# Optimization experiments

Hardware: AMD Instinct MI355X
Metric: run time of the kernel (lower is better)

Reference implementation:

```python
import jax, jax.numpy as jnp
import numpy as np

N_NODES = 100000


def setup_inputs() -> dict:
    key = jax.random.key(0)
    ks = jax.random.split(key, 4)
    x = jax.random.normal(ks[0], (N_NODES, 64), dtype=jnp.float32)
    edge_index = jax.random.randint(ks[1], (2, 1600000), 0, N_NODES, dtype=jnp.int64)
    # Glorot-ish scaled weights
    W1 = jax.random.normal(ks[2], (64, 64), dtype=jnp.float32) * (1.0 / np.sqrt(64))
    b1 = jnp.zeros((64,), dtype=jnp.float32)
    W2 = jax.random.normal(ks[3], (64, 19), dtype=jnp.float32) * (1.0 / np.sqrt(64))
    b2 = jnp.zeros((19,), dtype=jnp.float32)
    return {"x": x, "edge_index": edge_index, "W1": W1, "b1": b1, "W2": W2, "b2": b2}


def _gcn_norm(edge_index, num_nodes, dtype):
    # PyG gcn_norm: add self-loops (fill_value=1, improved=False), then
    # norm = deg^-1/2[src] * deg^-1/2[dst] with deg computed over destination.
    loops = jnp.arange(num_nodes, dtype=edge_index.dtype)
    src = jnp.concatenate([edge_index[0], loops])
    dst = jnp.concatenate([edge_index[1], loops])
    deg = jax.ops.segment_sum(jnp.ones_like(dst, dtype=dtype), dst, num_segments=num_nodes)
    dinv = jax.lax.rsqrt(deg)  # deg >= 1 thanks to self-loops
    norm = dinv[src] * dinv[dst]  # [E + N]
    return src, dst, norm


def _gcn_conv(h, src, dst, norm, W, b, num_nodes):
    hw = h @ W                                  # dense transform [N, d_out]
    msg = norm[:, None] * hw[src]               # gather + edge scaling [E+N, d_out]
    out = jax.ops.segment_sum(msg, dst, num_segments=num_nodes)  # scatter-add
    return out + b


def reference(x, edge_index, W1, b1, W2, b2):
    n = x.shape[0]
    src, dst, norm = _gcn_norm(edge_index, n, x.dtype)
    h = jax.nn.relu(_gcn_conv(x, src, dst, norm, W1, b1, n))
    # dropout is identity in eval mode (training=False)
    return _gcn_conv(h, src, dst, norm, W2, b2, n)
```

## Files before the change

### kernel.cpp

```cpp
#include <hip/hip_runtime.h>

#define TPB 256
#define BSH 5
#define BNODES 32
#define CAP 1024
#define EPB 8192
#define NBMAX 3200


__global__ void k_hist1(const int* __restrict__ dst, int* __restrict__ hist,
                        int nb, int E) {
    __shared__ int sh[NBMAX];
    int tid = threadIdx.x, blk = blockIdx.x;
    for (int i = tid; i < nb; i += TPB) sh[i] = 0;
    __syncthreads();
    int e0 = blk * EPB;
    for (int i = tid; i < EPB; i += TPB) {
        int e = e0 + i;
        if (e < E) atomicAdd(&sh[dst[e] >> BSH], 1);
    }
    __syncthreads();
    int* hrow = hist + (size_t)blk * nb;
    for (int i = tid; i < nb; i += TPB) hrow[i] = sh[i];
}

__global__ void k_scanoff(const int* __restrict__ hist, int* __restrict__ offs,
                          int* __restrict__ bcnt, int nblk, int nb) {
    int t = blockIdx.x * TPB + threadIdx.x;
    int b = t >> 3, s = t & 7;
    if (b >= nb) return;
    int nps = (nblk + 7) >> 3;
    int sum = 0;
    for (int q = 0; q < nps; ++q) {
        int blk = q * 8 + s;
        if (blk < nblk) sum += hist[(size_t)blk * nb + b];
    }
    int v = sum;
#pragma unroll
    for (int o = 1; o < 8; o <<= 1) {
        int u = __shfl_up(v, o, 8);
        if (s >= o) v += u;
    }
    int total = __shfl(v, 7, 8);
    if (s == 0) bcnt[b] = total;
    int off = b * CAP + (v - sum);
    for (int q = 0; q < nps; ++q) {
        int blk = q * 8 + s;
        if (blk < nblk) {
            offs[(size_t)blk * nb + b] = off;
            off += hist[(size_t)blk * nb + b];
        }
    }
}

__global__ void k_scatter(const int* __restrict__ src, const int* __restrict__ dst,
                          const int* __restrict__ offs, unsigned* __restrict__ ebuf,
                          int nb, int E) {
    __shared__ int cur[NBMAX];
    int tid = threadIdx.x, blk = blockIdx.x;
    const int* orow = offs + (size_t)blk * nb;
    for (int i = tid; i < nb; i += TPB) cur[i] = orow[i];
    __syncthreads();
    int e0 = blk * EPB;
    for (int i = tid; i < EPB; i += TPB) {
        int e = e0 + i;
        if (e < E) {
            int d = dst[e];
            int pos = atomicAdd(&cur[d >> BSH], 1);
            ebuf[pos] = ((unsigned)src[e] << BSH) | (unsigned)(d & (BNODES - 1));
        }
    }
}

__global__ void k_bcsr(const int* __restrict__ bcnt, const unsigned* __restrict__ ebuf,
                       int* __restrict__ csr, int* __restrict__ node_beg,
                       int* __restrict__ degi, float* __restrict__ dinv, int nb, int n) {
    __shared__ unsigned se[4][CAP];
    __shared__ int scnt[4][BNODES];
    __shared__ int sexc[4][BNODES];
    __shared__ int srnk[4][BNODES];
    int wv = threadIdx.x >> 6, lane = threadIdx.x & 63;
    int b = blockIdx.x * 4 + wv;
    bool act = (b < nb);
    if (lane < BNODES) { scnt[wv][lane] = 0; srnk[wv][lane] = 0; }
    __syncthreads();
    int cnt = 0;
    if (act) {
        cnt = bcnt[b];
        if (cnt > CAP) cnt = CAP;
        const unsigned* p = &ebuf[(size_t)b * CAP];
        for (int k = lane; k < cnt; k += 64) {
            unsigned pk = p[k];
            se[wv][k] = pk;
            atomicAdd(&scnt[wv][pk & (BNODES - 1)], 1);
        }
    }
    __syncthreads();
    if (act && lane < BNODES) {
        int dg = scnt[wv][lane];
        int v = dg;
#pragma unroll
        for (int off = 1; off < BNODES; off <<= 1) {
            int t = __shfl_up(v, off, BNODES);
            if (lane >= off) v += t;
        }
        int excl = v - dg;
        sexc[wv][lane] = excl;
        int node = b * BNODES + lane;
        if (node < n) {
            degi[node] = dg;
            node_beg[node] = b * CAP + excl;
            dinv[node] = rsqrtf((float)dg + 1.0f);
        }
    }
    __syncthreads();
    if (act) {
        int* csrb = csr + (size_t)b * CAP;
        for (int k = lane; k < cnt; k += 64) {
            unsigned pk = se[wv][k];
            int dl = pk & (BNODES - 1);
            int r = atomicAdd(&srnk[wv][dl], 1);
            csrb[sexc[wv][dl] + r] = (int)(pk >> BSH);
        }
    }
}


__global__ void k_xw64v(const float* __restrict__ x, const float* __restrict__ W,
                        const float* __restrict__ dinv, _Float16* __restrict__ g, int n) {
    __shared__ float Ws[64 * 64];
    __shared__ float xsT[64 * 64];
    int tid = threadIdx.x;
    int row0 = blockIdx.x * 64;
    for (int i = tid; i < 1024; i += TPB)
        reinterpret_cast<float4*>(Ws)[i] = reinterpret_cast<const float4*>(W)[i];
    {
        int rl = tid >> 2, cq = (tid & 3) * 16;
        int row = row0 + rl;
#pragma unroll
        for (int j4 = 0; j4 < 4; ++j4) {
            float4 v = make_float4(0.f, 0.f, 0.f, 0.f);
            if (row < n) v = *reinterpret_cast<const float4*>(x + (size_t)row * 64 + cq + j4 * 4);
            xsT[(cq + j4 * 4 + 0) * 64 + rl] = v.x;
            xsT[(cq + j4 * 4 + 1) * 64 + rl] = v.y;
            xsT[(cq + j4 * 4 + 2) * 64 + rl] = v.z;
            xsT[(cq + j4 * 4 + 3) * 64 + rl] = v.w;
        }
    }
    __syncthreads();
    int c4 = (tid & 15) * 4, rq = (tid >> 4) * 4;
    float acc[4][4] = {};
#pragma unroll 4
    for (int k = 0; k < 64; ++k) {
        float4 wv = *reinterpret_cast<const float4*>(Ws + k * 64 + c4);
        float4 xv = *reinterpret_cast<const float4*>(xsT + k * 64 + rq);
        const float* wp = (const float*)&wv;
        const float* xp = (const float*)&xv;
#pragma unroll
        for (int i = 0; i < 4; ++i)
#pragma unroll
            for (int j = 0; j < 4; ++j) acc[i][j] += xp[i] * wp[j];
    }
#pragma unroll
    for (int i = 0; i < 4; ++i) {
        int row = row0 + rq + i;
        if (row < n) {
            float dv = dinv[row];
            _Float16 o[4];
#pragma unroll
            for (int j = 0; j < 4; ++j) o[j] = (_Float16)(dv * acc[i][j]);
            *reinterpret_cast<ushort4*>(g + (size_t)row * 64 + c4) =
                *reinterpret_cast<const ushort4*>(o);
        }
    }
}

__global__ void k_xw19v(const _Float16* __restrict__ h, const float* __restrict__ W,
                        const float* __restrict__ dinv, _Float16* __restrict__ g2, int n) {
    __shared__ float Ws[64 * 32];
    __shared__ float xsT[64 * 32];
    int tid = threadIdx.x;
    int row0 = blockIdx.x * 32;
    for (int i = tid; i < 64 * 32; i += TPB) {
        int k = i >> 5, c = i & 31;
        Ws[i] = (c < 19) ? W[k * 19 + c] : 0.f;
    }
    {
        int rl = tid >> 3, sq = tid & 7;
        int row = row0 + rl;
        if (row < n) {
            uint4 v = *(reinterpret_cast<const uint4*>(h + (size_t)row * 64) + sq);
            const _Float16* f = (const _Float16*)&v;
#pragma unroll
            for (int j = 0; j < 8; ++j) xsT[(sq * 8 + j) * 32 + rl] = (float)f[j];
        } else {
#pragma unroll
            for (int j = 0; j < 8; ++j) xsT[(sq * 8 + j) * 32 + rl] = 0.f;
        }
    }
    __syncthreads();
    int c = tid & 31, rg = (tid >> 5) * 4;
    float acc[4] = {};
#pragma unroll 4
    for (int k = 0; k < 64; ++k) {
        float wv = Ws[k * 32 + c];
        float4 xv = *reinterpret_cast<const float4*>(xsT + k * 32 + rg);
        const float* xp = (const float*)&xv;
#pragma unroll
        for (int i = 0; i < 4; ++i) acc[i] += xp[i] * wv;
    }
    if (c < 19) {
#pragma unroll
        for (int i = 0; i < 4; ++i) {
            int row = row0 + rg + i;
            if (row < n) g2[(size_t)row * 19 + c] = (_Float16)(dinv[row] * acc[i]);
        }
    }
}


__global__ void k_gath64d(const int* __restrict__ node_beg, const int* __restrict__ degi,
                          const int* __restrict__ csr, const float* __restrict__ dinv,
                          const _Float16* __restrict__ g, const float* __restrict__ b1,
                          _Float16* __restrict__ h, int n) {
    int node = blockIdx.x * 4 + (threadIdx.x >> 6);
    if (node >= n) return;
    int lane = threadIdx.x & 63;
    int eidx = lane >> 3, fch = lane & 7;
    int beg = node_beg[node], cnt = degi[node];
    const uint4* gb = (const uint4*)g;
    float acc[8];
#pragma unroll
    for (int j = 0; j < 8; ++j) acc[j] = 0.f;
    for (int base = 0; base < cnt; base += 32) {
        int k0 = base + eidx, k1 = base + 8 + eidx;
        int k2 = base + 16 + eidx, k3 = base + 24 + eidx;
        bool v0 = (k0 < cnt), v1 = (k1 < cnt), v2 = (k2 < cnt), v3 = (k3 < cnt);
        int r0 = v0 ? csr[beg + k0] : 0;
        int r1 = v1 ? csr[beg + k1] : 0;
        int r2 = v2 ? csr[beg + k2] : 0;
        int r3 = v3 ? csr[beg + k3] : 0;
        uint4 A = v0 ? gb[(size_t)r0 * 8 + fch] : make_uint4(0, 0, 0, 0);
        uint4 B = v1 ? gb[(size_t)r1 * 8 + fch] : make_uint4(0, 0, 0, 0);
        uint4 C = v2 ? gb[(size_t)r2 * 8 + fch] : make_uint4(0, 0, 0, 0);
        uint4 D = v3 ? gb[(size_t)r3 * 8 + fch] : make_uint4(0, 0, 0, 0);
        const _Float16* fa = (const _Float16*)&A;
        const _Float16* fb = (const _Float16*)&B;
        const _Float16* fc = (const _Float16*)&C;
        const _Float16* fd = (const _Float16*)&D;
#pragma unroll
        for (int j = 0; j < 8; ++j)
            acc[j] += ((float)fa[j] + (float)fb[j]) + ((float)fc[j] + (float)fd[j]);
    }
#pragma unroll
    for (int m = 8; m < 64; m <<= 1) {
#pragma unroll
        for (int j = 0; j < 8; ++j) acc[j] += __shfl_xor(acc[j], m);
    }
    if (eidx == 0) {
        uint4 v = gb[(size_t)node * 8 + fch];
        const _Float16* f = (const _Float16*)&v;
        float dv = dinv[node];
        _Float16 outv[8];
#pragma unroll
        for (int j = 0; j < 8; ++j) {
            float val = dv * (acc[j] + (float)f[j]) + b1[fch * 8 + j];
            outv[j] = (_Float16)fmaxf(val, 0.f);
        }
        *((uint4*)(h + (size_t)node * 64) + fch) = *(const uint4*)outv;
    }
}

__global__ void k_gath19(const int* __restrict__ node_beg, const int* __restrict__ degi,
                         const int* __restrict__ csr, const float* __restrict__ dinv,
                         const _Float16* __restrict__ g2, const float* __restrict__ b2,
                         float* __restrict__ out, int n) {
    int node = blockIdx.x * 8 + (threadIdx.x >> 5);
    if (node >= n) return;
    int c = threadIdx.x & 31;
    if (c >= 19) return;
    int beg = node_beg[node], cnt = degi[node];
    float a0 = (float)g2[(size_t)node * 19 + c];
    float a1 = 0.f, a2 = 0.f, a3 = 0.f;
    float a4 = 0.f, a5 = 0.f, a6 = 0.f, a7 = 0.f;
    int k = 0;
    for (; k + 7 < cnt; k += 8) {
        int s0 = csr[beg + k];
        int s1 = csr[beg + k + 1];
        int s2 = csr[beg + k + 2];
        int s3 = csr[beg + k + 3];
        int s4 = csr[beg + k + 4];
        int s5 = csr[beg + k + 5];
        int s6 = csr[beg + k + 6];
        int s7 = csr[beg + k + 7];
        a0 += (float)g2[(size_t)s0 * 19 + c];
        a1 += (float)g2[(size_t)s1 * 19 + c];
        a2 += (float)g2[(size_t)s2 * 19 + c];
        a3 += (float)g2[(size_t)s3 * 19 + c];
        a4 += (float)g2[(size_t)s4 * 19 + c];
        a5 += (float)g2[(size_t)s5 * 19 + c];
        a6 += (float)g2[(size_t)s6 * 19 + c];
        a7 += (float)g2[(size_t)s7 * 19 + c];
    }
    for (; k < cnt; ++k) a1 += (float)g2[(size_t)csr[beg + k] * 19 + c];
    float s = ((a0 + a1) + (a2 + a3)) + ((a4 + a5) + (a6 + a7));
    out[(size_t)node * 19 + c] = dinv[node] * s + b2[c];
}


extern "C" void kernel_launch(void* const* d_in, const int* in_sizes, int n_in,
                              void* d_out, int out_size, void* d_ws, size_t ws_size,
                              hipStream_t stream) {
    const float* x  = (const float*)d_in[0];
    const int*   ei = (const int*)d_in[1];
    const float* W1 = (const float*)d_in[2];
    const float* b1 = (const float*)d_in[3];
    const float* W2 = (const float*)d_in[4];
    const float* b2 = (const float*)d_in[5];
    float* out = (float*)d_out;

    int N = in_sizes[0] / 64;
    int E = in_sizes[1] / 2;
    const int* src = ei;
    const int* dst = ei + E;

    int NB = (N + BNODES - 1) >> BSH;
    int NBLK = (E + EPB - 1) / EPB;

    char* w = (char*)d_ws;
    int* bcnt      = (int*)w;      w += (size_t)NB * 4;
    int* degi      = (int*)w;      w += (size_t)N * 4;
    int* node_beg  = (int*)w;      w += (size_t)N * 4;
    float* dinv    = (float*)w;    w += (size_t)N * 4;
    w = (char*)(((size_t)w + 63) & ~(size_t)63);
    char* regionA  = w;
    size_t histB   = (size_t)NBLK * NB * 4;
    size_t csrB    = (size_t)NB * CAP * 4;
    size_t regA    = (histB * 2 > csrB) ? histB * 2 : csrB;
    int* hist      = (int*)regionA;
    int* offs      = (int*)(regionA + histB);
    int* csr       = (int*)regionA;
    w += regA;
    unsigned* ebuf = (unsigned*)w; w += (size_t)NB * CAP * 4;
    _Float16* g1   = (_Float16*)w; w += (size_t)N * 64 * 2;
    _Float16* h    = (_Float16*)w; w += (size_t)N * 64 * 2;
    _Float16* g2   = g1;

    k_hist1   <<<NBLK, TPB, 0, stream>>>(dst, hist, NB, E);
    k_scanoff <<<(NB * 8 + TPB - 1) / TPB, TPB, 0, stream>>>(hist, offs, bcnt, NBLK, NB);
    k_scatter <<<NBLK, TPB, 0, stream>>>(src, dst, offs, ebuf, NB, E);
    k_bcsr    <<<(NB + 3) / 4, TPB, 0, stream>>>(bcnt, ebuf, csr, node_beg, degi, dinv, NB, N);

    k_xw64v   <<<(N + 63) / 64, TPB, 0, stream>>>(x, W1, dinv, g1, N);
    k_gath64d <<<(N + 3) / 4, TPB, 0, stream>>>(node_beg, degi, csr, dinv, g1, b1, h, N);

    k_xw19v   <<<(N + 31) / 32, TPB, 0, stream>>>(h, W2, dinv, g2, N);
    k_gath19  <<<(N + 7) / 8, TPB, 0, stream>>>(node_beg, degi, csr, dinv, g2, b2, out, N);
}
```

Baseline: 188.1 us.

## Pad layer-2 features to 20 halves and gather with wave-per-node packed loads

The second-layer transform now writes a row stride of 20 halves, zero-padding column 19. This lets each lane load a 4-byte pair of features. The layer-2 gather is restructured so one 64-lane wave handles a node: 6 edge slots × 10 feature pairs, with CSR indices loaded once per chunk and broadcast by shuffle, then a cross-lane reduction. Nontemporal loads are also added for streamed CSR and edge-buffer reads. The aim is fewer idle lanes and more coalesced gather traffic, at the cost of shuffle overhead and 4 unused lanes per wave.

```diff
diff --git a/kernel.cpp b/kernel.cpp
--- a/kernel.cpp
+++ b/kernel.cpp
@@ -90,7 +90,7 @@
         if (cnt > CAP) cnt = CAP;
         const unsigned* p = &ebuf[(size_t)b * CAP];
         for (int k = lane; k < cnt; k += 64) {
-            unsigned pk = p[k];
+            unsigned pk = __builtin_nontemporal_load(&p[k]);
             se[wv][k] = pk;
             atomicAdd(&scnt[wv][pk & (BNODES - 1)], 1);
         }
@@ -175,8 +175,8 @@
     }
 }
 
-__global__ void k_xw19v(const _Float16* __restrict__ h, const float* __restrict__ W,
-                        const float* __restrict__ dinv, _Float16* __restrict__ g2, int n) {
+__global__ void k_xw20v(const _Float16* __restrict__ h, const float* __restrict__ W,
+                        const float* __restrict__ dinv, _Float16* __restrict__ g2p, int n) {
     __shared__ float Ws[64 * 32];
     __shared__ float xsT[64 * 32];
     int tid = threadIdx.x;
@@ -209,11 +209,13 @@
 #pragma unroll
         for (int i = 0; i < 4; ++i) acc[i] += xp[i] * wv;
     }
-    if (c < 19) {
+    if (c < 20) {
 #pragma unroll
         for (int i = 0; i < 4; ++i) {
             int row = row0 + rg + i;
-            if (row < n) g2[(size_t)row * 19 + c] = (_Float16)(dinv[row] * acc[i]);
+            if (row < n)
+                g2p[(size_t)row * 20 + c] =
+                    (c < 19) ? (_Float16)(dinv[row] * acc[i]) : (_Float16)0.f;
         }
     }
 }
@@ -236,10 +238,10 @@
         int k0 = base + eidx, k1 = base + 8 + eidx;
         int k2 = base + 16 + eidx, k3 = base + 24 + eidx;
         bool v0 = (k0 < cnt), v1 = (k1 < cnt), v2 = (k2 < cnt), v3 = (k3 < cnt);
-        int r0 = v0 ? csr[beg + k0] : 0;
-        int r1 = v1 ? csr[beg + k1] : 0;
-        int r2 = v2 ? csr[beg + k2] : 0;
-        int r3 = v3 ? csr[beg + k3] : 0;
+        int r0 = v0 ? __builtin_nontemporal_load(&csr[beg + k0]) : 0;
+        int r1 = v1 ? __builtin_nontemporal_load(&csr[beg + k1]) : 0;
+        int r2 = v2 ? __builtin_nontemporal_load(&csr[beg + k2]) : 0;
+        int r3 = v3 ? __builtin_nontemporal_load(&csr[beg + k3]) : 0;
         uint4 A = v0 ? gb[(size_t)r0 * 8 + fch] : make_uint4(0, 0, 0, 0);
         uint4 B = v1 ? gb[(size_t)r1 * 8 + fch] : make_uint4(0, 0, 0, 0);
         uint4 C = v2 ? gb[(size_t)r2 * 8 + fch] : make_uint4(0, 0, 0, 0);
@@ -271,40 +273,50 @@
     }
 }
 
-__global__ void k_gath19(const int* __restrict__ node_beg, const int* __restrict__ degi,
-                         const int* __restrict__ csr, const float* __restrict__ dinv,
-                         const _Float16* __restrict__ g2, const float* __restrict__ b2,
-                         float* __restrict__ out, int n) {
-    int node = blockIdx.x * 8 + (threadIdx.x >> 5);
+__global__ void k_g19w(const int* __restrict__ node_beg, const int* __restrict__ degi,
+                       const int* __restrict__ csr, const float* __restrict__ dinv,
+                       const _Float16* __restrict__ g2p, const float* __restrict__ b2,
+                       float* __restrict__ out, int n) {
+    int node = blockIdx.x * 4 + (threadIdx.x >> 6);
     if (node >= n) return;
-    int c = threadIdx.x & 31;
-    if (c >= 19) return;
+    int lane = threadIdx.x & 63;
+    int e = lane / 10;
+    int cp = lane - e * 10;
+    bool act = (e < 6);
     int beg = node_beg[node], cnt = degi[node];
-    float a0 = (float)g2[(size_t)node * 19 + c];
-    float a1 = 0.f, a2 = 0.f, a3 = 0.f;
-    float a4 = 0.f, a5 = 0.f, a6 = 0.f, a7 = 0.f;
-    int k = 0;
-    for (; k + 7 < cnt; k += 8) {
-        int s0 = csr[beg + k];
-        int s1 = csr[beg + k + 1];
-        int s2 = csr[beg + k + 2];
-        int s3 = csr[beg + k + 3];
-        int s4 = csr[beg + k + 4];
-        int s5 = csr[beg + k + 5];
-        int s6 = csr[beg + k + 6];
-        int s7 = csr[beg + k + 7];
-        a0 += (float)g2[(size_t)s0 * 19 + c];
-        a1 += (float)g2[(size_t)s1 * 19 + c];
-        a2 += (float)g2[(size_t)s2 * 19 + c];
-        a3 += (float)g2[(size_t)s3 * 19 + c];
-        a4 += (float)g2[(size_t)s4 * 19 + c];
-        a5 += (float)g2[(size_t)s5 * 19 + c];
-        a6 += (float)g2[(size_t)s6 * 19 + c];
-        a7 += (float)g2[(size_t)s7 * 19 + c];
-    }
-    for (; k < cnt; ++k) a1 += (float)g2[(size_t)csr[beg + k] * 19 + c];
-    float s = ((a0 + a1) + (a2 + a3)) + ((a4 + a5) + (a6 + a7));
-    out[(size_t)node * 19 + c] = dinv[node] * s + b2[c];
+    const unsigned* gp = (const unsigned*)g2p;
+    float a0 = 0.f, a1 = 0.f;
+    for (int base = 0; base < cnt; base += 12) {
+        int cl = 0;
+        if (lane < 12 && base + lane < cnt)
+            cl = __builtin_nontemporal_load(&csr[beg + base + lane]);
+        int r0 = __shfl(cl, e);
+        int r1 = __shfl(cl, 6 + e);
+        bool v0 = act && (base + e < cnt);
+        bool v1 = act && (base + 6 + e < cnt);
+        unsigned u0 = v0 ? gp[(size_t)r0 * 10 + cp] : 0u;
+        unsigned u1 = v1 ? gp[(size_t)r1 * 10 + cp] : 0u;
+        const _Float16* h0 = (const _Float16*)&u0;
+        const _Float16* h1 = (const _Float16*)&u1;
+        a0 += (float)h0[0] + (float)h1[0];
+        a1 += (float)h0[1] + (float)h1[1];
+    }
+    float s0 = 0.f, s1 = 0.f;
+#pragma unroll
+    for (int eo = 0; eo < 6; ++eo) {
+        s0 += __shfl(a0, cp + eo * 10);
+        s1 += __shfl(a1, cp + eo * 10);
+    }
+    if (e == 0) {
+        unsigned su = gp[(size_t)node * 10 + cp];
+        const _Float16* sf = (const _Float16*)&su;
+        s0 += (float)sf[0];
+        s1 += (float)sf[1];
+        float dv = dinv[node];
+        int c0 = cp * 2;
+        out[(size_t)node * 19 + c0] = dv * s0 + b2[c0];
+        if (c0 + 1 < 19) out[(size_t)node * 19 + c0 + 1] = dv * s1 + b2[c0 + 1];
+    }
 }
 
 
@@ -344,7 +356,7 @@
     unsigned* ebuf = (unsigned*)w; w += (size_t)NB * CAP * 4;
     _Float16* g1   = (_Float16*)w; w += (size_t)N * 64 * 2;
     _Float16* h    = (_Float16*)w; w += (size_t)N * 64 * 2;
-    _Float16* g2   = g1;
+    _Float16* g2p  = g1;
 
     k_hist1   <<<NBLK, TPB, 0, stream>>>(dst, hist, NB, E);
     k_scanoff <<<(NB * 8 + TPB - 1) / TPB, TPB, 0, stream>>>(hist, offs, bcnt, NBLK, NB);
@@ -354,6 +366,6 @@
     k_xw64v   <<<(N + 63) / 64, TPB, 0, stream>>>(x, W1, dinv, g1, N);
     k_gath64d <<<(N + 3) / 4, TPB, 0, stream>>>(node_beg, degi, csr, dinv, g1, b1, h, N);
 
-    k_xw19v   <<<(N + 31) / 32, TPB, 0, stream>>>(h, W2, dinv, g2, N);
-    k_gath19  <<<(N + 7) / 8, TPB, 0, stream>>>(node_beg, degi, csr, dinv, g2, b2, out, N);
-}
+    k_xw20v   <<<(N + 31) / 32, TPB, 0, stream>>>(h, W2, dinv, g2p, N);
+    k_g19w    <<<(N + 3) / 4, TPB, 0, stream>>>(node_beg, degi, csr, dinv, g2p, b2, out, N);
+}
```

After: 210.7 us. +12.0%, slower.
